# Optimization experiments

Measured on AMD Instinct MI355X. Metric: run time of the kernel, lower is better.

The kernel has to match this reference:

```python
import jax, jax.numpy as jnp
import numpy as np

H = 12          # num_attention_heads
D = 64          # attention_head_size
HID = H * D     # hidden_size = 768
M = 1024        # max_position_embeddings


def setup_inputs() -> dict:
    key = jax.random.key(0)
    ks = jax.random.split(key, 9)
    B, S = 4, 1024
    s = 0.02
    return {
        "hidden_states": jax.random.normal(ks[0], (B, S, HID), jnp.float32),
        "attention_mask": jnp.zeros((B, 1, 1, S), jnp.float32),
        "Wq": jax.random.normal(ks[1], (HID, HID), jnp.float32) * s,
        "bq": jnp.zeros((HID,), jnp.float32),
        "Wk": jax.random.normal(ks[2], (HID, HID), jnp.float32) * s,
        "bk": jnp.zeros((HID,), jnp.float32),
        "Wv": jax.random.normal(ks[3], (HID, HID), jnp.float32) * s,
        "bv": jnp.zeros((HID,), jnp.float32),
        "dist_emb": jax.random.normal(ks[4], (2 * M - 1, D), jnp.float32) * s,
    }


def reference(hidden_states, attention_mask, Wq, bq, Wk, bk, Wv, bv, dist_emb):
    B, S, _ = hidden_states.shape

    def heads(x):  # [B,S,HID] -> [B,H,S,D]
        return x.reshape(B, S, H, D).transpose(0, 2, 1, 3)

    q = heads(hidden_states @ Wq + bq)
    k = heads(hidden_states @ Wk + bk)
    v = heads(hidden_states @ Wv + bv)

    # raw dot-product scores [B,H,S,S]
    scores = jnp.einsum('bhld,bhrd->bhlr', q, k)

    # relative_key_query positional bias
    pos = jnp.arange(S)
    distance = pos[:, None] - pos[None, :] + (M - 1)   # [S,S] in [0, 2M-2]
    pe = dist_emb[distance]                            # [S,S,D]
    scores = scores + jnp.einsum('bhld,lrd->bhlr', q, pe) \
                    + jnp.einsum('bhrd,lrd->bhlr', k, pe)

    scores = scores / jnp.sqrt(jnp.asarray(D, scores.dtype)) + attention_mask
    probs = jax.nn.softmax(scores, axis=-1)            # dropout is identity in eval

    ctx = jnp.einsum('bhlr,bhrd->bhld', probs, v)      # [B,H,S,D]
    ctx = ctx.transpose(0, 2, 1, 3).reshape(B, S, HID)
    return ctx, probs
```

## Files before the change

kernel.cpp:

```cpp
#include <hip/hip_runtime.h>
#include <hip/hip_bf16.h>

#define DEVFN __device__ __forceinline__

typedef __bf16 bf16x8 __attribute__((ext_vector_type(8)));
typedef float f32x4 __attribute__((ext_vector_type(4)));
typedef unsigned short ushort8 __attribute__((ext_vector_type(8)));
typedef unsigned short us4 __attribute__((ext_vector_type(4)));

namespace {

constexpr int S = 1024;
constexpr int HID = 768;
constexpr int NH = 12;
constexpr int HD = 64;

DEVFN unsigned short f2bf(float f) {
  union { float f; unsigned u; } v; v.f = f;
  unsigned r = v.u + 0x7FFF + ((v.u >> 16) & 1);
  return (unsigned short)(r >> 16);
}

DEVFN float bf2f(unsigned short u) {
  union { unsigned u; float f; } v; v.u = ((unsigned)u) << 16; return v.f;
}

DEVFN f32x4 zero4() { return f32x4{0.f, 0.f, 0.f, 0.f}; }

DEVFN f32x4 mfma_bf16(bf16x8 a, bf16x8 b, f32x4 c) {
  return __builtin_amdgcn_mfma_f32_16x16x32_bf16(a, b, c, 0, 0, 0);
}

DEVFN void gload16(void* lds_base, const void* gsrc) {
  __builtin_amdgcn_global_load_lds(
      (const __attribute__((address_space(1))) void*)gsrc,
      (__attribute__((address_space(3))) void*)lds_base, 16, 0, 0);
}

DEVFN bf16x8 frag_ld(const char* tile, int row, int ch) {
  int chs = ch ^ (row & 7);
  return *(const bf16x8*)(tile + row * 128 + chs * 16);
}

__global__ void k0_cvt_x(const float* __restrict__ x, unsigned short* __restrict__ xb) {
  size_t i = (size_t)(blockIdx.x * 256 + threadIdx.x) * 8;
  float4 a = *(const float4*)(x + i);
  float4 c = *(const float4*)(x + i + 4);
  ushort8 o;
  o[0] = f2bf(a.x); o[1] = f2bf(a.y); o[2] = f2bf(a.z); o[3] = f2bf(a.w);
  o[4] = f2bf(c.x); o[5] = f2bf(c.y); o[6] = f2bf(c.z); o[7] = f2bf(c.w);
  *(ushort8*)(xb + i) = o;
}

__global__ void k0_cvt_pe(const float* __restrict__ de, unsigned short* __restrict__ peb) {
  size_t i = (size_t)(blockIdx.x * 256 + threadIdx.x) * 8;
  int row = (int)(i >> 6);
  ushort8 o;
  if (row < 2047) {
    float4 a = *(const float4*)(de + i);
    float4 c = *(const float4*)(de + i + 4);
    o[0] = f2bf(a.x); o[1] = f2bf(a.y); o[2] = f2bf(a.z); o[3] = f2bf(a.w);
    o[4] = f2bf(c.x); o[5] = f2bf(c.y); o[6] = f2bf(c.z); o[7] = f2bf(c.w);
  } else {
    o = ushort8{0, 0, 0, 0, 0, 0, 0, 0};
  }
  *(ushort8*)(peb + i) = o;
}

__global__ __launch_bounds__(256) void k0_wt(const float* __restrict__ Wq,
                                             const float* __restrict__ Wk,
                                             const float* __restrict__ Wv,
                                             unsigned short* __restrict__ wt) {
  __shared__ float t[64][65];
  int bidx = blockIdx.x;
  int sec = bidx / 144, rem = bidx % 144;
  int ktb = rem / 12, ntb = rem % 12;
  const float* W = (sec == 0) ? Wq : ((sec == 1) ? Wk : Wv);
  int k0 = ktb * 64, n0 = ntb * 64;
  int tid = threadIdx.x;
  #pragma unroll
  for (int p = 0; p < 4; ++p) {
    int id = p * 256 + tid;
    int row = id >> 4, ch = id & 15;
    float4 v = *(const float4*)(W + (size_t)(k0 + row) * 768 + n0 + ch * 4);
    t[row][ch * 4 + 0] = v.x; t[row][ch * 4 + 1] = v.y;
    t[row][ch * 4 + 2] = v.z; t[row][ch * 4 + 3] = v.w;
  }
  __syncthreads();
  #pragma unroll
  for (int p = 0; p < 2; ++p) {
    int id = p * 256 + tid;
    int nrow = id >> 3, c8 = id & 7;
    ushort8 o;
    #pragma unroll
    for (int i = 0; i < 8; ++i) o[i] = f2bf(t[c8 * 8 + i][nrow]);
    *(ushort8*)(wt + (size_t)(sec * 768 + n0 + nrow) * 768 + k0 + c8 * 8) = o;
  }
}

__global__ __launch_bounds__(256) void k1_qkv(
    const unsigned short* __restrict__ xb, const unsigned short* __restrict__ wt,
    const float* __restrict__ bq, const float* __restrict__ bk, const float* __restrict__ bv,
    unsigned short* __restrict__ q_ws, unsigned short* __restrict__ k_ws,
    unsigned short* __restrict__ vt_ws) {
  __shared__ char ldsA[8192], ldsB[8192];
  const int tid = threadIdx.x, lane = tid & 63, wv = tid >> 6;
  const int row16 = lane & 15, cgrp = lane >> 4;
  const int ntb = blockIdx.x % 36, mtb = blockIdx.x / 36;
  const int sec = ntb / 12;
  const int n0 = ntb * 64;
  const int m0 = mtb * 64;

  f32x4 acc[4] = {zero4(), zero4(), zero4(), zero4()};

  for (int k0 = 0; k0 < 768; k0 += 64) {
    #pragma unroll
    for (int c = 0; c < 2; ++c) {
      int cc = (wv * 2 + c) * 64 + lane;
      int row = cc >> 3, ch = cc & 7, chs = ch ^ (row & 7);
      gload16(ldsA + (wv * 2 + c) * 1024, xb + (size_t)(m0 + row) * 768 + k0 + chs * 8);
      gload16(ldsB + (wv * 2 + c) * 1024, wt + (size_t)(n0 + row) * 768 + k0 + chs * 8);
    }
    __syncthreads();
    if (sec < 2) {
      bf16x8 af[2];
      #pragma unroll
      for (int k2 = 0; k2 < 2; ++k2) af[k2] = frag_ld(ldsA, wv * 16 + row16, k2 * 4 + cgrp);
      #pragma unroll
      for (int nt = 0; nt < 4; ++nt)
        #pragma unroll
        for (int k2 = 0; k2 < 2; ++k2) {
          bf16x8 bf = frag_ld(ldsB, nt * 16 + row16, k2 * 4 + cgrp);
          acc[nt] = mfma_bf16(af[k2], bf, acc[nt]);
        }
    } else {
      bf16x8 af[2];
      #pragma unroll
      for (int k2 = 0; k2 < 2; ++k2) af[k2] = frag_ld(ldsB, wv * 16 + row16, k2 * 4 + cgrp);
      #pragma unroll
      for (int mt = 0; mt < 4; ++mt)
        #pragma unroll
        for (int k2 = 0; k2 < 2; ++k2) {
          bf16x8 bx = frag_ld(ldsA, mt * 16 + row16, k2 * 4 + cgrp);
          acc[mt] = mfma_bf16(af[k2], bx, acc[mt]);
        }
    }
    __syncthreads();
  }

  if (sec < 2) {
    unsigned short* dst = (sec == 0) ? q_ws : k_ws;
    const float* bias = (sec == 0) ? bq : bk;
    int nl0 = (ntb % 12) * 64;
    #pragma unroll
    for (int nt = 0; nt < 4; ++nt) {
      int nn = nl0 + nt * 16 + row16;
      float bb = bias[nn];
      int hh = nn >> 6, dd = nn & 63;
      #pragma unroll
      for (int j = 0; j < 4; ++j) {
        int m = m0 + wv * 16 + cgrp * 4 + j;
        int b_ = m >> 10, s_ = m & 1023;
        dst[(size_t)((b_ * 12 + hh) * 1024 + s_) * 64 + dd] = f2bf(acc[nt][j] + bb);
      }
    }
  } else {
    int nl0 = (ntb % 12) * 64;
    #pragma unroll
    for (int j = 0; j < 4; ++j) {
      int nn = nl0 + wv * 16 + cgrp * 4 + j;
      float bb = bv[nn];
      int hh = nn >> 6, dd = nn & 63;
      #pragma unroll
      for (int mt = 0; mt < 4; ++mt) {
        int m = m0 + mt * 16 + row16;
        int b_ = m >> 10, s_ = m & 1023;
        vt_ws[(size_t)((b_ * 12 + hh) * 64 + dd) * 1024 + s_] = f2bf(acc[mt][j] + bb);
      }
    }
  }
}

__global__ __launch_bounds__(256) void kB_attn(
    const unsigned short* __restrict__ q_ws, const unsigned short* __restrict__ k_ws,
    const unsigned short* __restrict__ vt_ws, const unsigned short* __restrict__ peb,
    const float* __restrict__ mask, float* __restrict__ out_ctx,
    float* __restrict__ out_probs) {
  __shared__ __align__(16) unsigned short p_lds[16 * 1024];
  __shared__ __align__(16) unsigned short s3t[4][16 * 36];
  __shared__ __align__(16) unsigned short s2t[4][16 * 36];
  __shared__ __align__(16) float rsp[16][4];

  const int tid = threadIdx.x, lane = tid & 63, wv = tid >> 6;
  const int row16 = lane & 15, cgrp = lane >> 4;

  const int swz = (blockIdx.x & 7) * 384 + (blockIdx.x >> 3);
  const int qt = swz & 63, bh = swz >> 6;
  const int b = bh / NH, h = bh % NH;
  const int l0 = qt * 16;

  const unsigned short* qh = q_ws + (size_t)bh * S * HD;
  const unsigned short* khp = k_ws + (size_t)bh * S * HD;
  const unsigned short* vth = vt_ws + (size_t)bh * HD * S;
  const float* maskb = mask + b * S;

  bf16x8 qf[2];
  #pragma unroll
  for (int k2 = 0; k2 < 2; ++k2)
    qf[k2] = *(const bf16x8*)(qh + (size_t)(l0 + row16) * HD + k2 * 32 + cgrp * 8);

  unsigned short* s3w = &s3t[wv][0];
  unsigned short* s2w = &s2t[wv][0];
  float rs = 0.f;
  const int xsw = 2 * row16;

  auto loadK = [&](int rbase, bf16x8 (&kf)[2]) {
    #pragma unroll
    for (int k2 = 0; k2 < 2; ++k2)
      kf[k2] = *(const bf16x8*)(khp + (size_t)(rbase + row16) * HD + k2 * 32 + cgrp * 8);
  };
  auto loadPE = [&](int rbase, bf16x8 (&pef)[2][2]) {
    int pe0 = l0 - rbase + 1008;
    #pragma unroll
    for (int jt = 0; jt < 2; ++jt)
      #pragma unroll
      for (int k2 = 0; k2 < 2; ++k2)
        pef[jt][k2] = *(const bf16x8*)(peb + (size_t)(pe0 + jt * 16 + row16) * HD +
                                       k2 * 32 + cgrp * 8);
  };
  auto compute = [&](int rbase, const bf16x8 (&kf)[2], const bf16x8 (&pef)[2][2]) {
    #pragma unroll
    for (int jt = 0; jt < 2; ++jt) {
      f32x4 a = zero4();
      a = mfma_bf16(pef[jt][0], kf[0], a);
      a = mfma_bf16(pef[jt][1], kf[1], a);
      us4 o;
      o[0] = f2bf(a[0]); o[1] = f2bf(a[1]); o[2] = f2bf(a[2]); o[3] = f2bf(a[3]);
      *(us4*)(s3w + row16 * 36 + jt * 16 + cgrp * 4) = o;
    }
    #pragma unroll
    for (int jt = 0; jt < 2; ++jt) {
      f32x4 a = zero4();
      a = mfma_bf16(pef[jt][0], qf[0], a);
      a = mfma_bf16(pef[jt][1], qf[1], a);
      us4 o;
      o[0] = f2bf(a[0]); o[1] = f2bf(a[1]); o[2] = f2bf(a[2]); o[3] = f2bf(a[3]);
      *(us4*)(s2w + row16 * 36 + jt * 16 + cgrp * 4) = o;
    }
    f32x4 s1 = zero4();
    s1 = mfma_bf16(kf[0], qf[0], s1);
    s1 = mfma_bf16(kf[1], qf[1], s1);

    float4 mv = *(const float4*)(maskb + rbase + cgrp * 4);
    const float* mvp = (const float*)&mv;
    float pv[4];
    #pragma unroll
    for (int j = 0; j < 4; ++j) {
      int rl = cgrp * 4 + j;
      int jj = row16 - rl + 15;
      float b1 = bf2f(s2w[row16 * 36 + jj]);
      float b2 = bf2f(s3w[rl * 36 + jj]);
      float logit = (s1[j] + b1 + b2) * 0.125f + mvp[j];
      pv[j] = __expf(logit);
      rs += pv[j];
    }
    unsigned lo = (unsigned)f2bf(pv[0]) | ((unsigned)f2bf(pv[1]) << 16);
    unsigned hi = (unsigned)f2bf(pv[2]) | ((unsigned)f2bf(pv[3]) << 16);
    int c8 = (rbase >> 2) + cgrp;
    *(uint2*)((char*)p_lds + row16 * 2048 + (size_t)((c8 ^ xsw) * 8)) = uint2{lo, hi};
  };

  bf16x8 kfA[2], kfB[2], peA[2][2], peB[2][2];
  const int rb0 = wv * 16;
  loadK(rb0, kfA); loadPE(rb0, peA);
  #pragma unroll 1
  for (int rt2 = 0; rt2 < 8; ++rt2) {
    const int ra = rt2 * 128 + rb0;
    loadK(ra + 64, kfB); loadPE(ra + 64, peB);
    compute(ra, kfA, peA);
    if (rt2 < 7) { loadK(ra + 128, kfA); loadPE(ra + 128, peA); }
    compute(ra + 64, kfB, peB);
  }

  rs += __shfl_xor(rs, 16, 64);
  rs += __shfl_xor(rs, 32, 64);
  if (lane < 16) rsp[lane][wv] = rs;
  __syncthreads();

  f32x4 ctx0 = zero4(), ctx1 = zero4();
  #pragma unroll 4
  for (int ks = 0; ks < 32; ks += 2) {
    int c8a = ks * 8 + cgrp * 2;
    bf16x8 pa0 = *(const bf16x8*)((char*)p_lds + row16 * 2048 + (size_t)((c8a ^ xsw) * 8));
    bf16x8 pa1 = *(const bf16x8*)((char*)p_lds + row16 * 2048 +
                                  (size_t)(((c8a + 8) ^ xsw) * 8));
    bf16x8 vb0 = *(const bf16x8*)(vth + (size_t)(wv * 16 + row16) * S + ks * 32 + cgrp * 8);
    bf16x8 vb1 = *(const bf16x8*)(vth + (size_t)(wv * 16 + row16) * S + ks * 32 + 32 + cgrp * 8);
    ctx0 = mfma_bf16(pa0, vb0, ctx0);
    ctx1 = mfma_bf16(pa1, vb1, ctx1);
  }
  ctx0[0] += ctx1[0]; ctx0[1] += ctx1[1]; ctx0[2] += ctx1[2]; ctx0[3] += ctx1[3];

  #pragma unroll
  for (int j = 0; j < 4; ++j) {
    int l = cgrp * 4 + j;
    float4 r4 = *(const float4*)&rsp[l][0];
    float iv = 1.0f / (r4.x + r4.y + r4.z + r4.w);
    out_ctx[((size_t)(b * S + l0 + l)) * HID + h * HD + wv * 16 + row16] = ctx0[j] * iv;
  }

  {
    const int prow = tid >> 4, t = tid & 15;
    float4 r4 = *(const float4*)&rsp[prow][0];
    const float iv = 1.0f / (r4.x + r4.y + r4.z + r4.w);
    float* dst = out_probs + ((size_t)bh * S + l0 + prow) * S;
    const int xsr = 2 * prow;
    #pragma unroll
    for (int seg = 0; seg < 8; ++seg) {
      int cc = seg * 16 + t;
      ushort8 w = *(const ushort8*)((char*)p_lds + prow * 2048 +
                                    (size_t)((((cc * 2) ^ xsr)) * 8));
      float4 lo{bf2f(w[0]) * iv, bf2f(w[1]) * iv, bf2f(w[2]) * iv, bf2f(w[3]) * iv};
      float4 hi{bf2f(w[4]) * iv, bf2f(w[5]) * iv, bf2f(w[6]) * iv, bf2f(w[7]) * iv};
      *(float4*)(dst + cc * 8) = lo;
      *(float4*)(dst + cc * 8 + 4) = hi;
    }
  }
}

}

extern "C" void kernel_launch(void* const* d_in, const int* in_sizes, int n_in,
                              void* d_out, int out_size, void* d_ws, size_t ws_size,
                              hipStream_t stream) {
  const float* hidden = (const float*)d_in[0];
  const float* mask   = (const float*)d_in[1];
  const float* Wq = (const float*)d_in[2];
  const float* bq = (const float*)d_in[3];
  const float* Wk = (const float*)d_in[4];
  const float* bk = (const float*)d_in[5];
  const float* Wv = (const float*)d_in[6];
  const float* bv = (const float*)d_in[7];
  const float* de = (const float*)d_in[8];

  unsigned short* ws = (unsigned short*)d_ws;
  unsigned short* q_ws  = ws;
  unsigned short* k_ws  = ws + 3145728;
  unsigned short* vt_ws = ws + 6291456;
  unsigned short* xb    = ws + 9437184;
  unsigned short* wt    = ws + 12582912;
  unsigned short* peb   = ws + 14352384;

  float* outc = (float*)d_out;
  float* outp = outc + (size_t)4 * 1024 * 768;

  hipLaunchKernelGGL(k0_cvt_x, dim3(1536), dim3(256), 0, stream, hidden, xb);
  hipLaunchKernelGGL(k0_cvt_pe, dim3(64), dim3(256), 0, stream, de, peb);
  hipLaunchKernelGGL(k0_wt, dim3(432), dim3(256), 0, stream, Wq, Wk, Wv, wt);
  hipLaunchKernelGGL(k1_qkv, dim3(2304), dim3(256), 0, stream,
                     xb, wt, bq, bk, bv, q_ws, k_ws, vt_ws);
  hipLaunchKernelGGL(kB_attn, dim3(3072), dim3(256), 0, stream,
                     q_ws, k_ws, vt_ws, peb, mask, outc, outp);
}
```

Before: 234.3 us.

## Replace LDS staging of positional-bias tiles with register shuffles in attention kernel

The relative-position bias tiles (q·pe and k·pe) are no longer converted to bf16 and written to per-wave LDS scratch. They stay in MFMA accumulator registers and are gathered with lane rotations and cross-lane shuffles, which removes LDS round trips and a bf16 rounding step on the bias terms. The kernel also sets a launch-bounds occupancy hint, loads the mask via a helper, and rewrites the probs store loop to use 4-element chunks. The extra shuffles and selects add ALU and cross-lane work in the inner loop, and the occupancy hint may raise register pressure.

```diff
diff --git a/kernel.cpp b/kernel.cpp
--- a/kernel.cpp
+++ b/kernel.cpp
@@ -181,18 +181,16 @@
   }
 }
 
-__global__ __launch_bounds__(256) void kB_attn(
+__global__ __launch_bounds__(256, 4) void kC_attn(
     const unsigned short* __restrict__ q_ws, const unsigned short* __restrict__ k_ws,
     const unsigned short* __restrict__ vt_ws, const unsigned short* __restrict__ peb,
     const float* __restrict__ mask, float* __restrict__ out_ctx,
     float* __restrict__ out_probs) {
   __shared__ __align__(16) unsigned short p_lds[16 * 1024];
-  __shared__ __align__(16) unsigned short s3t[4][16 * 36];
-  __shared__ __align__(16) unsigned short s2t[4][16 * 36];
   __shared__ __align__(16) float rsp[16][4];
 
   const int tid = threadIdx.x, lane = tid & 63, wv = tid >> 6;
-  const int row16 = lane & 15, cgrp = lane >> 4;
+  const int l16 = lane & 15, cgrp = lane >> 4;
 
   const int swz = (blockIdx.x & 7) * 384 + (blockIdx.x >> 3);
   const int qt = swz & 63, bh = swz >> 6;
@@ -207,17 +205,16 @@
   bf16x8 qf[2];
   #pragma unroll
   for (int k2 = 0; k2 < 2; ++k2)
-    qf[k2] = *(const bf16x8*)(qh + (size_t)(l0 + row16) * HD + k2 * 32 + cgrp * 8);
-
-  unsigned short* s3w = &s3t[wv][0];
-  unsigned short* s2w = &s2t[wv][0];
+    qf[k2] = *(const bf16x8*)(qh + (size_t)(l0 + l16) * HD + k2 * 32 + cgrp * 8);
+
   float rs = 0.f;
-  const int xsw = 2 * row16;
+  const int xsw = 2 * l16;
+  const int jjbase = l16 + 15 - cgrp * 4;
 
   auto loadK = [&](int rbase, bf16x8 (&kf)[2]) {
     #pragma unroll
     for (int k2 = 0; k2 < 2; ++k2)
-      kf[k2] = *(const bf16x8*)(khp + (size_t)(rbase + row16) * HD + k2 * 32 + cgrp * 8);
+      kf[k2] = *(const bf16x8*)(khp + (size_t)(rbase + l16) * HD + k2 * 32 + cgrp * 8);
   };
   auto loadPE = [&](int rbase, bf16x8 (&pef)[2][2]) {
     int pe0 = l0 - rbase + 1008;
@@ -225,61 +222,75 @@
     for (int jt = 0; jt < 2; ++jt)
       #pragma unroll
       for (int k2 = 0; k2 < 2; ++k2)
-        pef[jt][k2] = *(const bf16x8*)(peb + (size_t)(pe0 + jt * 16 + row16) * HD +
+        pef[jt][k2] = *(const bf16x8*)(peb + (size_t)(pe0 + jt * 16 + l16) * HD +
                                        k2 * 32 + cgrp * 8);
   };
-  auto compute = [&](int rbase, const bf16x8 (&kf)[2], const bf16x8 (&pef)[2][2]) {
-    #pragma unroll
-    for (int jt = 0; jt < 2; ++jt) {
-      f32x4 a = zero4();
-      a = mfma_bf16(pef[jt][0], kf[0], a);
-      a = mfma_bf16(pef[jt][1], kf[1], a);
-      us4 o;
-      o[0] = f2bf(a[0]); o[1] = f2bf(a[1]); o[2] = f2bf(a[2]); o[3] = f2bf(a[3]);
-      *(us4*)(s3w + row16 * 36 + jt * 16 + cgrp * 4) = o;
-    }
-    #pragma unroll
-    for (int jt = 0; jt < 2; ++jt) {
-      f32x4 a = zero4();
-      a = mfma_bf16(pef[jt][0], qf[0], a);
-      a = mfma_bf16(pef[jt][1], qf[1], a);
-      us4 o;
-      o[0] = f2bf(a[0]); o[1] = f2bf(a[1]); o[2] = f2bf(a[2]); o[3] = f2bf(a[3]);
-      *(us4*)(s2w + row16 * 36 + jt * 16 + cgrp * 4) = o;
-    }
+  auto loadM = [&](int rbase) { return *(const float4*)(maskb + rbase + cgrp * 4); };
+
+  auto compute = [&](int rbase, const bf16x8 (&kf)[2], const bf16x8 (&pef)[2][2],
+                     float4 mv) {
+    f32x4 s3f0 = zero4(), s3f1 = zero4();
+    s3f0 = mfma_bf16(kf[0], pef[0][0], s3f0);
+    s3f0 = mfma_bf16(kf[1], pef[0][1], s3f0);
+    s3f1 = mfma_bf16(kf[0], pef[1][0], s3f1);
+    s3f1 = mfma_bf16(kf[1], pef[1][1], s3f1);
+    f32x4 s2f0 = zero4(), s2f1 = zero4();
+    s2f0 = mfma_bf16(pef[0][0], qf[0], s2f0);
+    s2f0 = mfma_bf16(pef[0][1], qf[1], s2f0);
+    s2f1 = mfma_bf16(pef[1][0], qf[0], s2f1);
+    s2f1 = mfma_bf16(pef[1][1], qf[1], s2f1);
     f32x4 s1 = zero4();
     s1 = mfma_bf16(kf[0], qf[0], s1);
     s1 = mfma_bf16(kf[1], qf[1], s1);
 
-    float4 mv = *(const float4*)(maskb + rbase + cgrp * 4);
+    const bool rb0 = (l16 & 1), rb1 = (l16 & 2);
+    float t0[4], t1[4], r0[4], r1[4];
+    #pragma unroll
+    for (int i = 0; i < 4; ++i) {
+      t0[i] = rb0 ? s2f0[(i + 1) & 3] : s2f0[i];
+      t1[i] = rb0 ? s2f1[(i + 1) & 3] : s2f1[i];
+    }
+    #pragma unroll
+    for (int i = 0; i < 4; ++i) {
+      r0[i] = rb1 ? t0[(i + 2) & 3] : t0[i];
+      r1[i] = rb1 ? t1[(i + 2) & 3] : t1[i];
+    }
+
     const float* mvp = (const float*)&mv;
     float pv[4];
     #pragma unroll
     for (int j = 0; j < 4; ++j) {
-      int rl = cgrp * 4 + j;
-      int jj = row16 - rl + 15;
-      float b1 = bf2f(s2w[row16 * 36 + jj]);
-      float b2 = bf2f(s3w[rl * 36 + jj]);
-      float logit = (s1[j] + b1 + b2) * 0.125f + mvp[j];
+      int jj = jjbase - j;
+      int j15 = jj & 15;
+      int src2 = ((j15 >> 2) << 4) | l16;
+      int src3 = (lane & 48) | j15;
+      float v20 = __shfl(r0[(3 - j) & 3], src2, 64);
+      float v21 = __shfl(r1[(3 - j) & 3], src2, 64);
+      float v30 = __shfl(s3f0[j], src3, 64);
+      float v31 = __shfl(s3f1[j], src3, 64);
+      bool hi = jj >= 16;
+      float b1v = hi ? v21 : v20;
+      float b2v = hi ? v31 : v30;
+      float logit = (s1[j] + b1v + b2v) * 0.125f + mvp[j];
       pv[j] = __expf(logit);
       rs += pv[j];
     }
     unsigned lo = (unsigned)f2bf(pv[0]) | ((unsigned)f2bf(pv[1]) << 16);
-    unsigned hi = (unsigned)f2bf(pv[2]) | ((unsigned)f2bf(pv[3]) << 16);
+    unsigned hiw = (unsigned)f2bf(pv[2]) | ((unsigned)f2bf(pv[3]) << 16);
     int c8 = (rbase >> 2) + cgrp;
-    *(uint2*)((char*)p_lds + row16 * 2048 + (size_t)((c8 ^ xsw) * 8)) = uint2{lo, hi};
+    *(uint2*)((char*)p_lds + l16 * 2048 + (size_t)((c8 ^ xsw) * 8)) = uint2{lo, hiw};
   };
 
   bf16x8 kfA[2], kfB[2], peA[2][2], peB[2][2];
-  const int rb0 = wv * 16;
-  loadK(rb0, kfA); loadPE(rb0, peA);
+  const int rbw = wv * 16;
+  loadK(rbw, kfA); loadPE(rbw, peA);
   #pragma unroll 1
   for (int rt2 = 0; rt2 < 8; ++rt2) {
-    const int ra = rt2 * 128 + rb0;
+    const int ra = rt2 * 128 + rbw;
     loadK(ra + 64, kfB); loadPE(ra + 64, peB);
-    compute(ra, kfA, peA);
+    compute(ra, kfA, peA, loadM(ra));
     if (rt2 < 7) { loadK(ra + 128, kfA); loadPE(ra + 128, peA); }
-    compute(ra + 64, kfB, peB);
+    compute(ra + 64, kfB, peB, loadM(ra + 64));
   }
 
   rs += __shfl_xor(rs, 16, 64);
@@ -291,11 +302,11 @@
   #pragma unroll 4
   for (int ks = 0; ks < 32; ks += 2) {
     int c8a = ks * 8 + cgrp * 2;
-    bf16x8 pa0 = *(const bf16x8*)((char*)p_lds + row16 * 2048 + (size_t)((c8a ^ xsw) * 8));
-    bf16x8 pa1 = *(const bf16x8*)((char*)p_lds + row16 * 2048 +
+    bf16x8 pa0 = *(const bf16x8*)((char*)p_lds + l16 * 2048 + (size_t)((c8a ^ xsw) * 8));
+    bf16x8 pa1 = *(const bf16x8*)((char*)p_lds + l16 * 2048 +
                                   (size_t)(((c8a + 8) ^ xsw) * 8));
-    bf16x8 vb0 = *(const bf16x8*)(vth + (size_t)(wv * 16 + row16) * S + ks * 32 + cgrp * 8);
-    bf16x8 vb1 = *(const bf16x8*)(vth + (size_t)(wv * 16 + row16) * S + ks * 32 + 32 + cgrp * 8);
+    bf16x8 vb0 = *(const bf16x8*)(vth + (size_t)(wv * 16 + l16) * S + ks * 32 + cgrp * 8);
+    bf16x8 vb1 = *(const bf16x8*)(vth + (size_t)(wv * 16 + l16) * S + ks * 32 + 32 + cgrp * 8);
     ctx0 = mfma_bf16(pa0, vb0, ctx0);
     ctx1 = mfma_bf16(pa1, vb1, ctx1);
   }
@@ -306,7 +317,7 @@
     int l = cgrp * 4 + j;
     float4 r4 = *(const float4*)&rsp[l][0];
     float iv = 1.0f / (r4.x + r4.y + r4.z + r4.w);
-    out_ctx[((size_t)(b * S + l0 + l)) * HID + h * HD + wv * 16 + row16] = ctx0[j] * iv;
+    out_ctx[((size_t)(b * S + l0 + l)) * HID + h * HD + wv * 16 + l16] = ctx0[j] * iv;
   }
 
   {
@@ -316,14 +327,11 @@
     float* dst = out_probs + ((size_t)bh * S + l0 + prow) * S;
     const int xsr = 2 * prow;
     #pragma unroll
-    for (int seg = 0; seg < 8; ++seg) {
-      int cc = seg * 16 + t;
-      ushort8 w = *(const ushort8*)((char*)p_lds + prow * 2048 +
-                                    (size_t)((((cc * 2) ^ xsr)) * 8));
-      float4 lo{bf2f(w[0]) * iv, bf2f(w[1]) * iv, bf2f(w[2]) * iv, bf2f(w[3]) * iv};
-      float4 hi{bf2f(w[4]) * iv, bf2f(w[5]) * iv, bf2f(w[6]) * iv, bf2f(w[7]) * iv};
-      *(float4*)(dst + cc * 8) = lo;
-      *(float4*)(dst + cc * 8 + 4) = hi;
+    for (int seg = 0; seg < 16; ++seg) {
+      int c = seg * 16 + t;
+      us4 w = *(const us4*)((char*)p_lds + prow * 2048 + (size_t)((c ^ xsr) * 8));
+      float4 o{bf2f(w[0]) * iv, bf2f(w[1]) * iv, bf2f(w[2]) * iv, bf2f(w[3]) * iv};
+      *(float4*)(dst + c * 4) = o;
     }
   }
 }
@@ -359,6 +367,6 @@
   hipLaunchKernelGGL(k0_wt, dim3(432), dim3(256), 0, stream, Wq, Wk, Wv, wt);
   hipLaunchKernelGGL(k1_qkv, dim3(2304), dim3(256), 0, stream,
                      xb, wt, bq, bk, bv, q_ws, k_ws, vt_ws);
-  hipLaunchKernelGGL(kB_attn, dim3(3072), dim3(256), 0, stream,
+  hipLaunchKernelGGL(kC_attn, dim3(3072), dim3(256), 0, stream,
                      q_ws, k_ws, vt_ws, peb, mask, outc, outp);
 }
```

Result: faster. 227.4 us (-3.0%).
